# Kernel optimization log

Hardware: AMD Instinct MI355X
Metric: run time of the kernel (lower is better)

Reference implementation:

```python
import jax, jax.numpy as jnp
import numpy as np

N = 4096
F_IN = 512
ALPHA = 0.2          # LeakyReLU negative slope
NEG_INF = -9e15      # mask fill used by pyGAT


def setup_inputs() -> dict:
    key = jax.random.key(0)
    ks = jax.random.split(key, 9)
    x = jax.random.normal(ks[0], (N, F_IN), dtype=jnp.float32)
    adj = (jax.random.uniform(ks[1], (N, N)) < 0.005).astype(jnp.float32)
    adj = jnp.maximum(adj, jnp.eye(N, dtype=jnp.float32))
    s = 0.05
    W1 = jax.random.normal(ks[2], (512, 8, 128), dtype=jnp.float32) * s
    a_src1 = jax.random.normal(ks[3], (8, 128), dtype=jnp.float32) * s
    a_dst1 = jax.random.normal(ks[4], (8, 128), dtype=jnp.float32) * s
    W2 = jax.random.normal(ks[5], (1024, 1, 16), dtype=jnp.float32) * s
    a_src2 = jax.random.normal(ks[6], (1, 16), dtype=jnp.float32) * s
    a_dst2 = jax.random.normal(ks[7], (1, 16), dtype=jnp.float32) * s
    return {"x": x, "adj": adj, "W1": W1, "a_src1": a_src1, "a_dst1": a_dst1,
            "W2": W2, "a_src2": a_src2, "a_dst2": a_dst2}


def gat_layer(x, mask, W, a_src, a_dst, concat, activation):
    # x: [N, Fin], W: [Fin, H, Fout]
    h = jnp.einsum('nf,fho->nho', x, W)                  # [N, H, Fout]
    f_src = jnp.einsum('nho,ho->hn', h, a_src)            # [H, N]
    f_dst = jnp.einsum('nho,ho->hn', h, a_dst)            # [H, N]
    e = f_src[:, :, None] + f_dst[:, None, :]             # [H, N, N]
    e = jax.nn.leaky_relu(e, ALPHA)
    e = jnp.where(mask[None, :, :], e, NEG_INF)
    attn = jax.nn.softmax(e, axis=-1)                     # masked softmax over neighbors j
    out = jnp.einsum('hij,jho->iho', attn, h)             # [N, H, Fout]
    if concat:
        out = out.reshape(out.shape[0], -1)               # [N, H*Fout]
    else:
        out = out.mean(axis=1)                            # [N, Fout]
    if activation:
        out = jax.nn.elu(out)
    return out


def reference(x, adj, W1, a_src1, a_dst1, W2, a_src2, a_dst2):
    mask = adj > 0
    h1 = gat_layer(x, mask, W1, a_src1, a_dst1, concat=True, activation=True)
    h2 = gat_layer(h1, mask, W2, a_src2, a_dst2, concat=False, activation=False)
    out = jax.nn.elu(h2)
    return jax.nn.log_softmax(out, axis=1)
```

## Files before the change

kernel.cpp:

```cpp
#include <hip/hip_runtime.h>
#include <hip/hip_bf16.h>

typedef __attribute__((ext_vector_type(8))) short short8;
typedef __attribute__((ext_vector_type(4))) float f32x4;

#define MAXNBR 128
#define ALPHA 0.2f

static __device__ __forceinline__ unsigned short f2bf(float f) {
    union { float f; unsigned u; } v; v.f = f;
    unsigned r = v.u + 0x7FFF + ((v.u >> 16) & 1);
    return (unsigned short)(r >> 16);
}
static __device__ __forceinline__ float bf2f(unsigned short u) {
    union { unsigned u; float f; } v; v.u = ((unsigned)u) << 16;
    return v.f;
}

__global__ __launch_bounds__(256) void cvt(const float* __restrict__ x,
                                           unsigned short* __restrict__ xb,
                                           const float* __restrict__ W1,
                                           unsigned short* __restrict__ W1t,
                                           const float* __restrict__ W2,
                                           unsigned short* __restrict__ W2b) {
    int b = blockIdx.x, t = threadIdx.x;
    if (b < 1024) {
        size_t base = (size_t)b * 2048 + t * 8;
        float4 v0 = *(const float4*)&x[base];
        float4 v1 = *(const float4*)&x[base + 4];
        short8 o;
        o[0] = f2bf(v0.x); o[1] = f2bf(v0.y); o[2] = f2bf(v0.z); o[3] = f2bf(v0.w);
        o[4] = f2bf(v1.x); o[5] = f2bf(v1.y); o[6] = f2bf(v1.z); o[7] = f2bf(v1.w);
        *(short8*)&xb[base] = o;
    } else if (b < 3072) {
        int idx = (b - 1024) * 256 + t;
        int c = idx >> 9, k = idx & 511;
        W1t[idx] = f2bf(W1[(size_t)k * 1024 + c]);
    } else {
        int idx = (b - 3072) * 256 + t;
        W2b[idx] = f2bf(W2[idx]);
    }
}

__global__ __launch_bounds__(256) void gemm_scan(const unsigned short* __restrict__ A,
                                                 const unsigned short* __restrict__ Bt,
                                                 unsigned short* __restrict__ C,
                                                 const float* __restrict__ adj,
                                                 int* __restrict__ nbr_idx,
                                                 int* __restrict__ nbr_cnt) {
    __shared__ unsigned short Asm[128 * 64];
    __shared__ unsigned short Bsm[64 * 64];
    int b = blockIdx.x;
    int tid = threadIdx.x;
    if (b < 512) {
        int lane = tid & 63;
        int w = tid >> 6;
        int wr = w >> 1, wc = w & 1;
        int rowBase = (b & 31) * 128, colBase = (b >> 5) * 64;
        int lr = lane >> 3;
        int lc = (lane & 7) * 8;
        f32x4 acc[4][2] = {};
        for (int k0 = 0; k0 < 512; k0 += 64) {
            #pragma unroll
            for (int i = 0; i < 4; ++i) {
                int rA = i * 32 + w * 8;
                __builtin_amdgcn_global_load_lds(
                    (const __attribute__((address_space(1))) void*)&A[(size_t)(rowBase + rA + lr) * 512 + k0 + lc],
                    (__attribute__((address_space(3))) void*)&Asm[rA * 64],
                    16, 0, 0);
            }
            #pragma unroll
            for (int i = 0; i < 2; ++i) {
                int rB = i * 32 + w * 8;
                __builtin_amdgcn_global_load_lds(
                    (const __attribute__((address_space(1))) void*)&Bt[(size_t)(colBase + rB + lr) * 512 + k0 + lc],
                    (__attribute__((address_space(3))) void*)&Bsm[rB * 64],
                    16, 0, 0);
            }
            __syncthreads();
            #pragma unroll
            for (int kk = 0; kk < 64; kk += 32) {
                short8 af[4], bfv[2];
                int kf = kk + (lane >> 4) * 8;
                #pragma unroll
                for (int m = 0; m < 4; ++m)
                    af[m] = *(const short8*)&Asm[(wr * 64 + m * 16 + (lane & 15)) * 64 + kf];
                #pragma unroll
                for (int n = 0; n < 2; ++n)
                    bfv[n] = *(const short8*)&Bsm[(wc * 32 + n * 16 + (lane & 15)) * 64 + kf];
                #pragma unroll
                for (int m = 0; m < 4; ++m)
                    #pragma unroll
                    for (int n = 0; n < 2; ++n)
                        acc[m][n] = __builtin_amdgcn_mfma_f32_16x16x32_bf16(af[m], bfv[n], acc[m][n], 0, 0, 0);
            }
            __syncthreads();
        }
        int crow0 = rowBase + wr * 64, ccol0 = colBase + wc * 32;
        #pragma unroll
        for (int m = 0; m < 4; ++m)
            #pragma unroll
            for (int n = 0; n < 2; ++n) {
                int col = ccol0 + n * 16 + (lane & 15);
                int row0 = crow0 + m * 16 + (lane >> 4) * 4;
                #pragma unroll
                for (int r = 0; r < 4; ++r)
                    C[(size_t)(row0 + r) * 1024 + col] = f2bf(acc[m][n][r]);
            }
    } else {
        int row = (b - 512) * 4 + (tid >> 6);
        int lane = tid & 63;
        const float* arow = adj + (size_t)row * 4096;
        int cnt = 0;
        for (int base = 0; base < 4096; base += 256) {
            float4 v = *(const float4*)&arow[base + lane * 4];
            #pragma unroll
            for (int s = 0; s < 4; ++s) {
                float xv = ((const float*)&v)[s];
                unsigned long long m = __ballot(xv > 0.f);
                if (xv > 0.f) {
                    int pos = cnt + (int)__popcll(m & ((1ull << lane) - 1ull));
                    if (pos < MAXNBR) nbr_idx[row * MAXNBR + pos] = base + lane * 4 + s;
                }
                cnt += (int)__popcll(m);
            }
        }
        if (lane == 0) nbr_cnt[row] = cnt < MAXNBR ? cnt : MAXNBR;
    }
}

__global__ __launch_bounds__(256) void attn_coef1(const unsigned short* __restrict__ h1b,
                                                  const float* __restrict__ a_src,
                                                  const float* __restrict__ a_dst,
                                                  float* __restrict__ f_src,
                                                  float* __restrict__ f_dst) {
    int n = blockIdx.x, t = threadIdx.x;
    ushort4 v = *(const ushort4*)&h1b[(size_t)n * 1024 + t * 4];
    int head = t >> 5;
    int o0 = (t * 4) & 127;
    float hv0 = bf2f(v.x), hv1 = bf2f(v.y), hv2 = bf2f(v.z), hv3 = bf2f(v.w);
    float ps = hv0 * a_src[head * 128 + o0] + hv1 * a_src[head * 128 + o0 + 1]
             + hv2 * a_src[head * 128 + o0 + 2] + hv3 * a_src[head * 128 + o0 + 3];
    float pd = hv0 * a_dst[head * 128 + o0] + hv1 * a_dst[head * 128 + o0 + 1]
             + hv2 * a_dst[head * 128 + o0 + 2] + hv3 * a_dst[head * 128 + o0 + 3];
    #pragma unroll
    for (int off = 1; off < 32; off <<= 1) {
        ps += __shfl_xor(ps, off);
        pd += __shfl_xor(pd, off);
    }
    if ((t & 31) == 0) {
        f_src[head * 4096 + n] = ps;
        f_dst[head * 4096 + n] = pd;
    }
}

__global__ __launch_bounds__(256) void aggregate_fused(const unsigned short* __restrict__ h1b,
                                                       const int* __restrict__ nbr_idx,
                                                       const int* __restrict__ nbr_cnt,
                                                       const float* __restrict__ f_src,
                                                       const float* __restrict__ f_dst,
                                                       const unsigned short* __restrict__ W2b,
                                                       const float* __restrict__ a_src2,
                                                       const float* __restrict__ a_dst2,
                                                       float* __restrict__ h2,
                                                       float* __restrict__ f_src2,
                                                       float* __restrict__ f_dst2) {
    __shared__ int nbr[MAXNBR];
    __shared__ float attw[8][MAXNBR];
    __shared__ float fs[8];
    __shared__ float hrow[1024];
    __shared__ float partial[16][16];
    int i = blockIdx.x;
    int t = threadIdx.x;
    int cnt = nbr_cnt[i];
    if (t < MAXNBR) nbr[t] = (t < cnt) ? nbr_idx[i * MAXNBR + t] : 0;
    if (t < 8) fs[t] = f_src[t * 4096 + i];
    __syncthreads();
    {
        int h = t >> 5, sl = t & 31;
        float fsh = fs[h];
        float e[4];
        #pragma unroll
        for (int q = 0; q < 4; ++q) {
            int j = sl + q * 32;
            if (j < cnt) {
                float xv = fsh + f_dst[h * 4096 + nbr[j]];
                e[q] = xv > 0.f ? xv : ALPHA * xv;
            } else e[q] = -INFINITY;
        }
        float m = fmaxf(fmaxf(e[0], e[1]), fmaxf(e[2], e[3]));
        #pragma unroll
        for (int off = 1; off < 32; off <<= 1) m = fmaxf(m, __shfl_xor(m, off));
        float wq[4];
        float s = 0.f;
        #pragma unroll
        for (int q = 0; q < 4; ++q) {
            wq[q] = (e[q] == -INFINITY) ? 0.f : __expf(e[q] - m);
            s += wq[q];
        }
        #pragma unroll
        for (int off = 1; off < 32; off <<= 1) s += __shfl_xor(s, off);
        float inv = 1.f / s;
        #pragma unroll
        for (int q = 0; q < 4; ++q) attw[h][sl + q * 32] = wq[q] * inv;
    }
    __syncthreads();
    int h = t >> 5;
    const unsigned short* src = h1b + t * 4;
    float a0 = 0.f, a1 = 0.f, a2 = 0.f, a3 = 0.f;
    int cntPad = (cnt + 7) & ~7;
    for (int j = 0; j < cntPad; j += 8) {
        int4 nb0 = *(const int4*)&nbr[j];
        int4 nb1 = *(const int4*)&nbr[j + 4];
        float4 w0 = *(const float4*)&attw[h][j];
        float4 w1 = *(const float4*)&attw[h][j + 4];
        ushort4 v0 = *(const ushort4*)&src[(size_t)nb0.x << 10];
        ushort4 v1 = *(const ushort4*)&src[(size_t)nb0.y << 10];
        ushort4 v2 = *(const ushort4*)&src[(size_t)nb0.z << 10];
        ushort4 v3 = *(const ushort4*)&src[(size_t)nb0.w << 10];
        ushort4 v4 = *(const ushort4*)&src[(size_t)nb1.x << 10];
        ushort4 v5 = *(const ushort4*)&src[(size_t)nb1.y << 10];
        ushort4 v6 = *(const ushort4*)&src[(size_t)nb1.z << 10];
        ushort4 v7 = *(const ushort4*)&src[(size_t)nb1.w << 10];
        a0 += w0.x * bf2f(v0.x) + w0.y * bf2f(v1.x) + w0.z * bf2f(v2.x) + w0.w * bf2f(v3.x)
            + w1.x * bf2f(v4.x) + w1.y * bf2f(v5.x) + w1.z * bf2f(v6.x) + w1.w * bf2f(v7.x);
        a1 += w0.x * bf2f(v0.y) + w0.y * bf2f(v1.y) + w0.z * bf2f(v2.y) + w0.w * bf2f(v3.y)
            + w1.x * bf2f(v4.y) + w1.y * bf2f(v5.y) + w1.z * bf2f(v6.y) + w1.w * bf2f(v7.y);
        a2 += w0.x * bf2f(v0.z) + w0.y * bf2f(v1.z) + w0.z * bf2f(v2.z) + w0.w * bf2f(v3.z)
            + w1.x * bf2f(v4.z) + w1.y * bf2f(v5.z) + w1.z * bf2f(v6.z) + w1.w * bf2f(v7.z);
        a3 += w0.x * bf2f(v0.w) + w0.y * bf2f(v1.w) + w0.z * bf2f(v2.w) + w0.w * bf2f(v3.w)
            + w1.x * bf2f(v4.w) + w1.y * bf2f(v5.w) + w1.z * bf2f(v6.w) + w1.w * bf2f(v7.w);
    }
    a0 = a0 > 0.f ? a0 : expm1f(a0);
    a1 = a1 > 0.f ? a1 : expm1f(a1);
    a2 = a2 > 0.f ? a2 : expm1f(a2);
    a3 = a3 > 0.f ? a3 : expm1f(a3);
    *(float4*)&hrow[t * 4] = make_float4(a0, a1, a2, a3);
    __syncthreads();
    {
        int o = t & 15, seg = t >> 4;
        float acc = 0.f;
        #pragma unroll 8
        for (int k = seg * 64; k < seg * 64 + 64; ++k)
            acc += hrow[k] * bf2f(W2b[k * 16 + o]);
        partial[seg][o] = acc;
    }
    __syncthreads();
    if (t < 16) {
        float s2 = 0.f;
        #pragma unroll
        for (int g = 0; g < 16; ++g) s2 += partial[g][t];
        h2[i * 16 + t] = s2;
        float ps = s2 * a_src2[t];
        float pd = s2 * a_dst2[t];
        #pragma unroll
        for (int off = 1; off < 16; off <<= 1) {
            ps += __shfl_xor(ps, off);
            pd += __shfl_xor(pd, off);
        }
        if (t == 0) { f_src2[i] = ps; f_dst2[i] = pd; }
    }
}

__global__ __launch_bounds__(64) void final_layer(const float* __restrict__ h2,
                                                  const int* __restrict__ nbr_idx,
                                                  const int* __restrict__ nbr_cnt,
                                                  const float* __restrict__ f_src2,
                                                  const float* __restrict__ f_dst2,
                                                  float* __restrict__ out) {
    __shared__ float attn[MAXNBR];
    __shared__ int nbr[MAXNBR];
    int i = blockIdx.x;
    int l = threadIdx.x;
    int cnt = nbr_cnt[i];
    float fsi = f_src2[i];
    for (int j = l; j < MAXNBR; j += 64) {
        float e = -INFINITY;
        if (j < cnt) {
            int jj = nbr_idx[i * MAXNBR + j];
            nbr[j] = jj;
            float xv = fsi + f_dst2[jj];
            e = xv > 0.f ? xv : ALPHA * xv;
        }
        attn[j] = e;
    }
    __syncthreads();
    float m = fmaxf(attn[l], attn[l + 64]);
    #pragma unroll
    for (int off = 1; off < 64; off <<= 1) m = fmaxf(m, __shfl_xor(m, off));
    float s = 0.f;
    {
        float e0 = attn[l], e1 = attn[l + 64];
        if (e0 != -INFINITY) s += __expf(e0 - m);
        if (e1 != -INFINITY) s += __expf(e1 - m);
    }
    #pragma unroll
    for (int off = 1; off < 64; off <<= 1) s += __shfl_xor(s, off);
    for (int j = l; j < MAXNBR; j += 64) {
        float e = attn[j];
        attn[j] = (e == -INFINITY) ? 0.f : __expf(e - m) / s;
    }
    __syncthreads();
    if (l < 16) {
        float acc = 0.f;
        for (int j = 0; j < cnt; ++j)
            acc += attn[j] * h2[nbr[j] * 16 + l];
        float v = acc > 0.f ? acc : expm1f(acc);
        float mx = v;
        #pragma unroll
        for (int off = 1; off < 16; off <<= 1) mx = fmaxf(mx, __shfl_xor(mx, off));
        float se = __expf(v - mx);
        #pragma unroll
        for (int off = 1; off < 16; off <<= 1) se += __shfl_xor(se, off);
        out[i * 16 + l] = v - mx - logf(se);
    }
}

extern "C" void kernel_launch(void* const* d_in, const int* in_sizes, int n_in,
                              void* d_out, int out_size, void* d_ws, size_t ws_size,
                              hipStream_t stream) {
    const float* x      = (const float*)d_in[0];
    const float* adj    = (const float*)d_in[1];
    const float* W1     = (const float*)d_in[2];
    const float* a_src1 = (const float*)d_in[3];
    const float* a_dst1 = (const float*)d_in[4];
    const float* W2     = (const float*)d_in[5];
    const float* a_src2 = (const float*)d_in[6];
    const float* a_dst2 = (const float*)d_in[7];
    float* out = (float*)d_out;

    char* ws = (char*)d_ws;
    unsigned short* xb    = (unsigned short*)ws;
    unsigned short* w1t   = (unsigned short*)(ws + (4u << 20));
    unsigned short* w2b   = (unsigned short*)(ws + (5u << 20));
    unsigned short* h1b   = (unsigned short*)(ws + (6u << 20));
    float* fsrc1 = (float*)(ws + (14u << 20));
    float* fdst1 = (float*)(ws + (14u << 20) + (128u << 10));
    float* h2    = (float*)(ws + (15u << 20));
    float* fsrc2 = (float*)(ws + (15u << 20) + (256u << 10));
    float* fdst2 = (float*)(ws + (15u << 20) + (272u << 10));
    int* nbr_idx = (int*)(ws + (16u << 20));
    int* nbr_cnt = (int*)(ws + (18u << 20));

    cvt<<<3136, 256, 0, stream>>>(x, xb, W1, w1t, W2, w2b);
    gemm_scan<<<1536, 256, 0, stream>>>(xb, w1t, h1b, adj, nbr_idx, nbr_cnt);
    attn_coef1<<<4096, 256, 0, stream>>>(h1b, a_src1, a_dst1, fsrc1, fdst1);
    aggregate_fused<<<4096, 256, 0, stream>>>(h1b, nbr_idx, nbr_cnt, fsrc1, fdst1,
                                              w2b, a_src2, a_dst2, h2, fsrc2, fdst2);
    final_layer<<<4096, 64, 0, stream>>>(h2, nbr_idx, nbr_cnt, fsrc2, fdst2, out);
}
```

Measured before the change: 71.18 us.

## Split layer-1 aggregation into per-head-pair wave blocks with a separate reduction kernel

The 256-thread-per-node aggregation kernel becomes four 64-thread blocks per node, each handling two heads, and writes partial layer-2 projections to a workspace. A new coef2 kernel sums the four partials and computes the layer-2 attention coefficients. W2 is now read directly in fp32 with vectorized loads, so its bf16 conversion is dropped from cvt. The aim is finer-grained parallelism and fewer block-wide barriers per node. The cost is an extra kernel launch, extra partial-sum traffic through global memory, and the neighbor list being loaded once per quarter block instead of once per node.

Measured after the change: 88.77 us. 1.25x slower.

```diff
diff --git a/kernel.cpp b/kernel.cpp
--- a/kernel.cpp
+++ b/kernel.cpp
@@ -20,9 +20,7 @@
 __global__ __launch_bounds__(256) void cvt(const float* __restrict__ x,
                                            unsigned short* __restrict__ xb,
                                            const float* __restrict__ W1,
-                                           unsigned short* __restrict__ W1t,
-                                           const float* __restrict__ W2,
-                                           unsigned short* __restrict__ W2b) {
+                                           unsigned short* __restrict__ W1t) {
     int b = blockIdx.x, t = threadIdx.x;
     if (b < 1024) {
         size_t base = (size_t)b * 2048 + t * 8;
@@ -32,13 +30,10 @@
         o[0] = f2bf(v0.x); o[1] = f2bf(v0.y); o[2] = f2bf(v0.z); o[3] = f2bf(v0.w);
         o[4] = f2bf(v1.x); o[5] = f2bf(v1.y); o[6] = f2bf(v1.z); o[7] = f2bf(v1.w);
         *(short8*)&xb[base] = o;
-    } else if (b < 3072) {
+    } else {
         int idx = (b - 1024) * 256 + t;
         int c = idx >> 9, k = idx & 511;
         W1t[idx] = f2bf(W1[(size_t)k * 1024 + c]);
-    } else {
-        int idx = (b - 3072) * 256 + t;
-        W2b[idx] = f2bf(W2[idx]);
     }
 }
 
@@ -154,39 +149,37 @@
     }
 }
 
-__global__ __launch_bounds__(256) void aggregate_fused(const unsigned short* __restrict__ h1b,
-                                                       const int* __restrict__ nbr_idx,
-                                                       const int* __restrict__ nbr_cnt,
-                                                       const float* __restrict__ f_src,
-                                                       const float* __restrict__ f_dst,
-                                                       const unsigned short* __restrict__ W2b,
-                                                       const float* __restrict__ a_src2,
-                                                       const float* __restrict__ a_dst2,
-                                                       float* __restrict__ h2,
-                                                       float* __restrict__ f_src2,
-                                                       float* __restrict__ f_dst2) {
+__global__ __launch_bounds__(64) void aggregate2(const unsigned short* __restrict__ h1b,
+                                                 const int* __restrict__ nbr_idx,
+                                                 const int* __restrict__ nbr_cnt,
+                                                 const float* __restrict__ f_src,
+                                                 const float* __restrict__ f_dst,
+                                                 const float* __restrict__ W2,
+                                                 float* __restrict__ h2part) {
     __shared__ int nbr[MAXNBR];
-    __shared__ float attw[8][MAXNBR];
-    __shared__ float fs[8];
-    __shared__ float hrow[1024];
-    __shared__ float partial[16][16];
-    int i = blockIdx.x;
+    __shared__ float attw[2][MAXNBR];
+    __shared__ float pored[64][17];
+    int bid = blockIdx.x;
+    int q = bid & 3;
+    int i = bid >> 2;
     int t = threadIdx.x;
     int cnt = nbr_cnt[i];
-    if (t < MAXNBR) nbr[t] = (t < cnt) ? nbr_idx[i * MAXNBR + t] : 0;
-    if (t < 8) fs[t] = f_src[t * 4096 + i];
-    __syncthreads();
+    nbr[t]      = (t < cnt)      ? nbr_idx[i * MAXNBR + t]      : 0;
+    nbr[t + 64] = (t + 64 < cnt) ? nbr_idx[i * MAXNBR + t + 64] : 0;
+    __syncthreads();
+    int hl = t >> 5;
+    int h = q * 2 + hl;
     {
-        int h = t >> 5, sl = t & 31;
-        float fsh = fs[h];
+        int sl = t & 31;
+        float fsh = f_src[h * 4096 + i];
         float e[4];
         #pragma unroll
-        for (int q = 0; q < 4; ++q) {
-            int j = sl + q * 32;
+        for (int p = 0; p < 4; ++p) {
+            int j = sl + p * 32;
             if (j < cnt) {
                 float xv = fsh + f_dst[h * 4096 + nbr[j]];
-                e[q] = xv > 0.f ? xv : ALPHA * xv;
-            } else e[q] = -INFINITY;
+                e[p] = xv > 0.f ? xv : ALPHA * xv;
+            } else e[p] = -INFINITY;
         }
         float m = fmaxf(fmaxf(e[0], e[1]), fmaxf(e[2], e[3]));
         #pragma unroll
@@ -194,26 +187,25 @@
         float wq[4];
         float s = 0.f;
         #pragma unroll
-        for (int q = 0; q < 4; ++q) {
-            wq[q] = (e[q] == -INFINITY) ? 0.f : __expf(e[q] - m);
-            s += wq[q];
+        for (int p = 0; p < 4; ++p) {
+            wq[p] = (e[p] == -INFINITY) ? 0.f : __expf(e[p] - m);
+            s += wq[p];
         }
         #pragma unroll
         for (int off = 1; off < 32; off <<= 1) s += __shfl_xor(s, off);
         float inv = 1.f / s;
         #pragma unroll
-        for (int q = 0; q < 4; ++q) attw[h][sl + q * 32] = wq[q] * inv;
-    }
-    __syncthreads();
-    int h = t >> 5;
-    const unsigned short* src = h1b + t * 4;
+        for (int p = 0; p < 4; ++p) attw[hl][sl + p * 32] = wq[p] * inv;
+    }
+    __syncthreads();
+    const unsigned short* src = h1b + q * 256 + t * 4;
     float a0 = 0.f, a1 = 0.f, a2 = 0.f, a3 = 0.f;
     int cntPad = (cnt + 7) & ~7;
     for (int j = 0; j < cntPad; j += 8) {
         int4 nb0 = *(const int4*)&nbr[j];
         int4 nb1 = *(const int4*)&nbr[j + 4];
-        float4 w0 = *(const float4*)&attw[h][j];
-        float4 w1 = *(const float4*)&attw[h][j + 4];
+        float4 w0 = *(const float4*)&attw[hl][j];
+        float4 w1 = *(const float4*)&attw[hl][j + 4];
         ushort4 v0 = *(const ushort4*)&src[(size_t)nb0.x << 10];
         ushort4 v1 = *(const ushort4*)&src[(size_t)nb0.y << 10];
         ushort4 v2 = *(const ushort4*)&src[(size_t)nb0.z << 10];
@@ -235,31 +227,60 @@
     a1 = a1 > 0.f ? a1 : expm1f(a1);
     a2 = a2 > 0.f ? a2 : expm1f(a2);
     a3 = a3 > 0.f ? a3 : expm1f(a3);
-    *(float4*)&hrow[t * 4] = make_float4(a0, a1, a2, a3);
-    __syncthreads();
+    float po[16];
     {
-        int o = t & 15, seg = t >> 4;
-        float acc = 0.f;
+        int f0 = q * 256 + t * 4;
+        float4 wr0 = *(const float4*)&W2[(size_t)(f0 + 0) * 16];
+        float4 wr1 = *(const float4*)&W2[(size_t)(f0 + 0) * 16 + 4];
+        float4 wr2 = *(const float4*)&W2[(size_t)(f0 + 0) * 16 + 8];
+        float4 wr3 = *(const float4*)&W2[(size_t)(f0 + 0) * 16 + 12];
+        po[0] = a0 * wr0.x; po[1] = a0 * wr0.y; po[2] = a0 * wr0.z; po[3] = a0 * wr0.w;
+        po[4] = a0 * wr1.x; po[5] = a0 * wr1.y; po[6] = a0 * wr1.z; po[7] = a0 * wr1.w;
+        po[8] = a0 * wr2.x; po[9] = a0 * wr2.y; po[10] = a0 * wr2.z; po[11] = a0 * wr2.w;
+        po[12] = a0 * wr3.x; po[13] = a0 * wr3.y; po[14] = a0 * wr3.z; po[15] = a0 * wr3.w;
+        float vr[3] = {a1, a2, a3};
+        #pragma unroll
+        for (int r = 1; r < 4; ++r) {
+            float4 u0 = *(const float4*)&W2[(size_t)(f0 + r) * 16];
+            float4 u1 = *(const float4*)&W2[(size_t)(f0 + r) * 16 + 4];
+            float4 u2 = *(const float4*)&W2[(size_t)(f0 + r) * 16 + 8];
+            float4 u3 = *(const float4*)&W2[(size_t)(f0 + r) * 16 + 12];
+            float v = vr[r - 1];
+            po[0] += v * u0.x; po[1] += v * u0.y; po[2] += v * u0.z; po[3] += v * u0.w;
+            po[4] += v * u1.x; po[5] += v * u1.y; po[6] += v * u1.z; po[7] += v * u1.w;
+            po[8] += v * u2.x; po[9] += v * u2.y; po[10] += v * u2.z; po[11] += v * u2.w;
+            po[12] += v * u3.x; po[13] += v * u3.y; po[14] += v * u3.z; po[15] += v * u3.w;
+        }
+    }
+    #pragma unroll
+    for (int o = 0; o < 16; ++o) pored[t][o] = po[o];
+    __syncthreads();
+    if (t < 16) {
+        float s = 0.f;
         #pragma unroll 8
-        for (int k = seg * 64; k < seg * 64 + 64; ++k)
-            acc += hrow[k] * bf2f(W2b[k * 16 + o]);
-        partial[seg][o] = acc;
-    }
-    __syncthreads();
-    if (t < 16) {
-        float s2 = 0.f;
-        #pragma unroll
-        for (int g = 0; g < 16; ++g) s2 += partial[g][t];
-        h2[i * 16 + t] = s2;
-        float ps = s2 * a_src2[t];
-        float pd = s2 * a_dst2[t];
-        #pragma unroll
-        for (int off = 1; off < 16; off <<= 1) {
-            ps += __shfl_xor(ps, off);
-            pd += __shfl_xor(pd, off);
-        }
-        if (t == 0) { f_src2[i] = ps; f_dst2[i] = pd; }
-    }
+        for (int k = 0; k < 64; ++k) s += pored[k][t];
+        h2part[(size_t)(q * 4096 + i) * 16 + t] = s;
+    }
+}
+
+__global__ __launch_bounds__(256) void coef2(const float* __restrict__ h2part,
+                                             const float* __restrict__ a_src2,
+                                             const float* __restrict__ a_dst2,
+                                             float* __restrict__ h2,
+                                             float* __restrict__ f_src2,
+                                             float* __restrict__ f_dst2) {
+    int idx = blockIdx.x * 256 + threadIdx.x;
+    int i = idx >> 4, o = idx & 15;
+    float s = h2part[idx] + h2part[65536 + idx] + h2part[131072 + idx] + h2part[196608 + idx];
+    h2[idx] = s;
+    float ps = s * a_src2[o];
+    float pd = s * a_dst2[o];
+    #pragma unroll
+    for (int off = 1; off < 16; off <<= 1) {
+        ps += __shfl_xor(ps, off);
+        pd += __shfl_xor(pd, off);
+    }
+    if (o == 0) { f_src2[i] = ps; f_dst2[i] = pd; }
 }
 
 __global__ __launch_bounds__(64) void final_layer(const float* __restrict__ h2,
@@ -332,7 +353,6 @@
     char* ws = (char*)d_ws;
     unsigned short* xb    = (unsigned short*)ws;
     unsigned short* w1t   = (unsigned short*)(ws + (4u << 20));
-    unsigned short* w2b   = (unsigned short*)(ws + (5u << 20));
     unsigned short* h1b   = (unsigned short*)(ws + (6u << 20));
     float* fsrc1 = (float*)(ws + (14u << 20));
     float* fdst1 = (float*)(ws + (14u << 20) + (128u << 10));
@@ -341,11 +361,12 @@
     float* fdst2 = (float*)(ws + (15u << 20) + (272u << 10));
     int* nbr_idx = (int*)(ws + (16u << 20));
     int* nbr_cnt = (int*)(ws + (18u << 20));
-
-    cvt<<<3136, 256, 0, stream>>>(x, xb, W1, w1t, W2, w2b);
+    float* h2part = (float*)(ws + (19u << 20));
+
+    cvt<<<3072, 256, 0, stream>>>(x, xb, W1, w1t);
     gemm_scan<<<1536, 256, 0, stream>>>(xb, w1t, h1b, adj, nbr_idx, nbr_cnt);
     attn_coef1<<<4096, 256, 0, stream>>>(h1b, a_src1, a_dst1, fsrc1, fdst1);
-    aggregate_fused<<<4096, 256, 0, stream>>>(h1b, nbr_idx, nbr_cnt, fsrc1, fdst1,
-                                              w2b, a_src2, a_dst2, h2, fsrc2, fdst2);
+    aggregate2<<<16384, 64, 0, stream>>>(h1b, nbr_idx, nbr_cnt, fsrc1, fdst1, W2, h2part);
+    coef2<<<256, 256, 0, stream>>>(h2part, a_src2, a_dst2, h2, fsrc2, fdst2);
     final_layer<<<4096, 64, 0, stream>>>(h2, nbr_idx, nbr_cnt, fsrc2, fdst2, out);
 }
```
